# Kernel optimization log

Hardware: AMD Instinct MI355X
Metric: run time of the kernel (lower is better)

## Reference

```python
import jax, jax.numpy as jnp
import numpy as np

N_ATOMS = 20
N_IN, N_EMB_N, N_EMB_E, N_H_N, N_H_E = 4, 128, 128, 256, 256


def lstm_seq(x, Wi, bi, Wh, bh):
    """x: [B, M, T, D] -> h sequence [B, M, T, H]. Gates stacked as (i,f,g,o).
    Equivalent to the per-gate nn.Linear pairs: bi/bh are the two bias vectors."""
    B, M, T, D = x.shape
    H = Wh.shape[0]
    # precompute all input-to-hidden projections in one big GEMM: [T,B,M,4H]
    xg = jnp.einsum('bmtd,dg->tbmg', x, Wi) + bi

    def step(carry, xg_t):
        c, h = carry
        g = xg_t + h @ Wh + bh  # [B,M,4H]
        i, f, gg, o = jnp.split(g, 4, axis=-1)
        i = jax.nn.sigmoid(i)
        f = jax.nn.sigmoid(f)
        gg = jnp.tanh(gg)
        o = jax.nn.sigmoid(o)
        c = f * c + i * gg
        h = o * jnp.tanh(c)
        return (c, h), h

    z = jnp.zeros((B, M, H), x.dtype)
    _, hs = jax.lax.scan(step, (z, z), xg)  # hs: [T,B,M,H]
    return jnp.transpose(hs, (1, 2, 0, 3))


def setup_inputs() -> dict:
    key = jax.random.key(0)
    ks = jax.random.split(key, 16)
    s = 0.05
    # fully-connected directed edges without self loops -> one-hot incidence
    send, rec = np.where(~np.eye(N_ATOMS, dtype=bool))
    eye = np.eye(N_ATOMS, dtype=np.float32)
    inp = {
        'X': jax.random.normal(ks[0], (16, N_ATOMS, 64, N_IN), jnp.float32),
        'rel_rec': jnp.asarray(eye[rec]),
        'rel_send': jnp.asarray(eye[send]),
        # motion embedding fc
        'Wm': jax.random.normal(ks[1], (N_IN, N_EMB_N), jnp.float32) * s,
        'bm': jnp.zeros((N_EMB_N,), jnp.float32),
        # motion LSTM (gates i,f,g,o stacked)
        'Wmi': jax.random.normal(ks[2], (N_EMB_N, 4 * N_H_N), jnp.float32) * s,
        'bmi': jnp.zeros((4 * N_H_N,), jnp.float32),
        'Wmh': jax.random.normal(ks[3], (N_H_N, 4 * N_H_N), jnp.float32) * s,
        'bmh': jnp.zeros((4 * N_H_N,), jnp.float32),
        # interaction embedding fc (in = 2*n_h_node)
        'We': jax.random.normal(ks[4], (2 * N_H_N, N_EMB_E), jnp.float32) * s,
        'be': jnp.zeros((N_EMB_E,), jnp.float32),
        # edge LSTM
        'Wei': jax.random.normal(ks[5], (N_EMB_E, 4 * N_H_E), jnp.float32) * s,
        'bei': jnp.zeros((4 * N_H_E,), jnp.float32),
        'Weh': jax.random.normal(ks[6], (N_H_E, 4 * N_H_E), jnp.float32) * s,
        'beh': jnp.zeros((4 * N_H_E,), jnp.float32),
        # output fc
        'Wf': jax.random.normal(ks[7], (N_H_E, 1), jnp.float32) * s,
        'bf': jnp.zeros((1,), jnp.float32),
    }
    return inp


def reference(X, rel_rec, rel_send, Wm, bm, Wmi, bmi, Wmh, bmh,
              We, be, Wei, bei, Weh, beh, Wf, bf):
    # Motion embedding on temporal deltas: [B,N,T-1,n_emb_node]
    dX = X[:, :, 1:, :] - X[:, :, :-1, :]
    em = dX @ Wm + bm
    # Motion LSTM, full sequence: [B,N,T-1,Hn]
    hm = lstm_seq(em, Wmi, bmi, Wmh, bmh)
    # Interaction embedding: gather per-edge sender/receiver node states
    senders = jnp.einsum('en,bnth->beth', rel_send, hm)
    receivers = jnp.einsum('en,bnth->beth', rel_rec, hm)
    edges = jnp.concatenate([senders, receivers], axis=-1)  # [B,E,T-1,2Hn]
    ea = edges @ We + be  # [B,E,T-1,n_emb_edge]
    # Edge LSTM, last hidden state: [B,E,He]
    he = lstm_seq(ea, Wei, bei, Weh, beh)[:, :, -1, :]
    # Edge scores -> dense adjacency via incidence matrices
    A = jax.nn.sigmoid(he @ Wf + bf)[..., 0]  # [B,E]
    Ad = jnp.einsum('en,be,em->bnm', rel_send, A, rel_rec)  # send^T diag(A) rec
    return 0.5 * (Ad + jnp.transpose(Ad, (0, 2, 1)))  # symmetrize
```

## Files before the change

kernel.cpp:

```cpp
#include <hip/hip_runtime.h>
#include <stdint.h>

#define NBATCH 16
#define NNODE  20
#define TSTEPS 63
#define NEDGE  380
#define HID    256
#define RS     280

typedef __bf16 bf16x8 __attribute__((ext_vector_type(8)));
typedef float  f32x4  __attribute__((ext_vector_type(4)));

__device__ __forceinline__ float bf2f(unsigned short u){
  union { unsigned int i; float f; } v; v.i = ((unsigned int)u) << 16; return v.f;
}
__device__ __forceinline__ unsigned short f2bf(float f){
  union { float f; unsigned int i; } v; v.f = f;
  return (unsigned short)((v.i + 0x7FFFu + ((v.i >> 16) & 1u)) >> 16);
}
__device__ __forceinline__ bf16x8 as_frag(uint4 v){
  union { uint4 u; bf16x8 b; } c; c.u = v; return c.b;
}
__device__ __forceinline__ float sigmf(float x){ return 1.0f/(1.0f+__expf(-x)); }
__device__ __forceinline__ float tanh_f(float x){ float e=__expf(2.0f*x); return (e-1.0f)/(e+1.0f); }

__device__ __forceinline__ unsigned long long load_ax(const unsigned long long* p){
  return __hip_atomic_load(p, __ATOMIC_RELAXED, __HIP_MEMORY_SCOPE_AGENT);
}
__device__ __forceinline__ void store_ax(unsigned long long* p, unsigned long long v){
  __hip_atomic_store(p, v, __ATOMIC_RELAXED, __HIP_MEMORY_SCOPE_AGENT);
}
__device__ __forceinline__ void wait_vm0(){ asm volatile("s_waitcnt vmcnt(0)" ::: "memory"); }

__device__ __forceinline__ void xpose4(f32x4& v, int cl){
  float s0 = __shfl_xor((float)v[1], 1), s1 = __shfl_xor((float)v[0], 1);
  float s2 = __shfl_xor((float)v[3], 1), s3 = __shfl_xor((float)v[2], 1);
  bool b0 = (cl & 1);
  float a0 = b0 ? s0 : v[0], a1 = b0 ? v[1] : s1;
  float a2 = b0 ? s2 : v[2], a3 = b0 ? v[3] : s3;
  float t0 = __shfl_xor(a2, 2), t1 = __shfl_xor(a3, 2);
  float t2 = __shfl_xor(a0, 2), t3 = __shfl_xor(a1, 2);
  bool b1 = (cl & 2);
  v[0] = b1 ? t0 : a0; v[1] = b1 ? t1 : a1;
  v[2] = b1 ? a2 : t2; v[3] = b1 ? a3 : t3;
}

__global__ __launch_bounds__(256) void prep_a(
    const float* __restrict__ We, const float* __restrict__ Wei,
    const float* __restrict__ Wm, const float* __restrict__ Wmi,
    const float* __restrict__ bm, const float* __restrict__ bmi, const float* __restrict__ bmh,
    const float* __restrict__ be, const float* __restrict__ bei, const float* __restrict__ beh,
    float* __restrict__ Wse, float* __restrict__ Wre, float* __restrict__ WcmGI,
    float* __restrict__ bcmGI, float* __restrict__ bceGI,
    float* __restrict__ Afin, unsigned int* __restrict__ ectr, unsigned int* __restrict__ mctr){
  int bid = blockIdx.x, tid = threadIdx.x;
  if (bid < 2048){
    int idx = bid*256 + tid;
    int half = idx >> 18;
    int j = idx & 262143;
    int k = j >> 10, nn = j & 1023;
    const float* Wrow = We + (half*256 + k)*128;
    float s = 0.f;
    for (int d = 0; d < 128; ++d) s += Wrow[d] * Wei[d*1024 + nn];
    (half ? Wre : Wse)[k*1024 + nn] = s;
  } else if (bid < 2064){
    int idx = (bid-2048)*256 + tid;
    int d = idx >> 10, ci = idx & 1023;
    int col = (ci & 3)*256 + (ci >> 2);
    float s = 0.f;
    for (int j = 0; j < 128; ++j) s += Wm[d*128 + j] * Wmi[j*1024 + col];
    WcmGI[idx] = s;
  } else if (bid < 2068){
    int ci = (bid-2064)*256 + tid;
    int col = (ci & 3)*256 + (ci >> 2);
    float s = bmi[col] + bmh[col];
    for (int j = 0; j < 128; ++j) s += bm[j] * Wmi[j*1024 + col];
    bcmGI[ci] = s;
  } else if (bid < 2072){
    int ci = (bid-2068)*256 + tid;
    int col = (ci & 3)*256 + (ci >> 2);
    float s = bei[col] + beh[col];
    for (int j = 0; j < 128; ++j) s += be[j] * Wei[j*1024 + col];
    bceGI[ci] = s;
  } else if (bid == 2072){
    for (int i = tid; i < 2048; i += 256) ectr[i] = 0u;
    for (int i = tid; i < 1024; i += 256) mctr[i] = 0u;
  } else {
    int idx = (bid-2073)*256 + tid;
    if (idx < NBATCH*NEDGE) Afin[idx] = 0.f;
  }
}

__device__ __forceinline__ void pack_gi(const float* __restrict__ W,
                                        unsigned short* __restrict__ dst, int id){
  int lane = id & 63, kt = (id >> 6) & 7, tt = (id >> 9) & 1, w = (id >> 10) & 7, nb = id >> 13;
  int cl = lane & 15, q = lane >> 4;
  int gcol = (cl & 3)*256 + nb*64 + (w*2 + tt)*4 + (cl >> 2);
  int k0 = kt*32 + q*8;
  unsigned int wb[4];
  #pragma unroll
  for (int p = 0; p < 4; ++p){
    unsigned short a = f2bf(W[(k0+2*p  )*1024 + gcol]);
    unsigned short b = f2bf(W[(k0+2*p+1)*1024 + gcol]);
    wb[p] = (unsigned int)a | ((unsigned int)b << 16);
  }
  ((uint4*)dst)[id] = make_uint4(wb[0], wb[1], wb[2], wb[3]);
}

__device__ __forceinline__ void pack_one(const float* __restrict__ S,
                                         unsigned short* __restrict__ dst, int id, int n){
  int lane = id & 63, kt = (id >> 6) & 7;
  int k0 = kt*32 + ((lane >> 4) << 3);
  unsigned int wb[4];
  #pragma unroll
  for (int p = 0; p < 4; ++p){
    unsigned short a = f2bf(S[(k0+2*p  )*1024 + n]);
    unsigned short b = f2bf(S[(k0+2*p+1)*1024 + n]);
    wb[p] = (unsigned int)a | ((unsigned int)b << 16);
  }
  ((uint4*)dst)[id] = make_uint4(wb[0], wb[1], wb[2], wb[3]);
}

__global__ __launch_bounds__(256) void prep_b(
    const float* __restrict__ Wmh, const float* __restrict__ Weh,
    const float* __restrict__ Wse, const float* __restrict__ Wre,
    unsigned short* __restrict__ pWmh, unsigned short* __restrict__ pWeh,
    unsigned short* __restrict__ pWsr){
  int gid = blockIdx.x*256 + threadIdx.x;
  if (gid < 32768){
    pack_gi(Wmh, pWmh, gid);
  } else if (gid < 65536){
    pack_gi(Weh, pWeh, gid - 32768);
  } else {
    int id = gid - 65536;
    int ng = (id >> 9)*16 + (id & 15);
    const float* S = (ng < 1024) ? Wse : Wre;
    pack_one(S, pWsr, id, ng & 1023);
  }
}

__global__ __launch_bounds__(512, 2) void motion_lstm(
    const float* __restrict__ X, const float* __restrict__ WcmGI,
    const float* __restrict__ bcmGI, const unsigned short* __restrict__ pWmh,
    unsigned short* __restrict__ hm, unsigned short* __restrict__ mb,
    unsigned int* __restrict__ mctr){
  __shared__ __align__(16) unsigned short hst[16*RS];
  __shared__ float dxs[10*252];
  __shared__ __align__(16) float sWc[4*256];
  __shared__ __align__(16) float sbc[256];
  int tid = threadIdx.x, lane = tid & 63, w = tid >> 6;
  int l15 = lane & 15, quad = lane >> 4;
  int m = blockIdx.x & 31, n = blockIdx.x >> 5;
  int s0 = m*10;
  unsigned int* ctr = mctr + m*32;

  uint4 wreg[2][8];
  #pragma unroll
  for (int tt = 0; tt < 2; ++tt)
    #pragma unroll
    for (int kt = 0; kt < 8; ++kt)
      wreg[tt][kt] = ((const uint4*)pWmh)[(((n*8 + w)*2 + tt)*8 + kt)*64 + lane];

  uint4 z4 = make_uint4(0,0,0,0);
  for (int i = tid; i < 560; i += 512) ((uint4*)hst)[i] = z4;
  for (int i = tid; i < 1024; i += 512) sWc[i] = WcmGI[(i >> 8)*1024 + n*256 + (i & 255)];
  if (tid < 256) sbc[tid] = bcmGI[n*256 + tid];
  for (int i = tid; i < 2520; i += 512){
    int sl = i / 252; int r = i % 252; int t = r >> 2; int d = r & 3;
    const float* Xp = X + (((size_t)(s0 + sl)*64 + t)*4 + d);
    dxs[i] = Xp[4] - Xp[0];
  }
  __syncthreads();

  float bb[2] = { sbc[(w*2+0)*16 + l15], sbc[(w*2+1)*16 + l15] };
  int row = quad*4 + (l15 & 3);
  int hsub = l15 >> 2;
  int slr = row < 10 ? row : 9;
  float ce[2] = {0.f, 0.f};

  for (int t = 0; t < TSTEPS; ++t){
    if (t > 0){
      if (tid == 0){
        unsigned int tgt = 4u*(unsigned)t;
        while (__hip_atomic_load(ctr, __ATOMIC_RELAXED, __HIP_MEMORY_SCOPE_AGENT) < tgt)
          __builtin_amdgcn_s_sleep(1);
      }
      __syncthreads();
      const unsigned long long* mbp = (const unsigned long long*)mb
          + ((size_t)((t-1)&1)*32 + m)*16*64;
      unsigned long long pv[2]; int po[2] = {-1,-1};
      #pragma unroll
      for (int j = 0; j < 2; ++j){
        int i = tid + j*512;
        if (i < 768){
          int which = i >> 8, jj = i & 255;
          int r = jj >> 4, c = jj & 15;
          int np = which + (which >= n ? 1 : 0);
          pv[j] = load_ax(&mbp[(size_t)r*64 + np*16 + c]);
          po[j] = r*RS + np*64 + c*4;
        }
      }
      #pragma unroll
      for (int j = 0; j < 2; ++j)
        if (po[j] >= 0) *(unsigned long long*)&hst[po[j]] = pv[j];
    }
    __syncthreads();

    f32x4 acc[2];
    acc[0] = (f32x4){bb[0],bb[0],bb[0],bb[0]};
    acc[1] = (f32x4){bb[1],bb[1],bb[1],bb[1]};
    #pragma unroll
    for (int kt = 0; kt < 8; ++kt){
      bf16x8 a = as_frag(*(const uint4*)&hst[l15*RS + kt*32 + quad*8]);
      acc[0] = __builtin_amdgcn_mfma_f32_16x16x32_bf16(a, as_frag(wreg[0][kt]), acc[0], 0, 0, 0);
      acc[1] = __builtin_amdgcn_mfma_f32_16x16x32_bf16(a, as_frag(wreg[1][kt]), acc[1], 0, 0, 0);
    }
    __syncthreads();

    f32x4 dxv = *(const f32x4*)&dxs[slr*252 + t*4];
    #pragma unroll
    for (int tt = 0; tt < 2; ++tt){
      int tl = w*2 + tt;
      f32x4 v = acc[tt];
      xpose4(v, l15);
      #pragma unroll
      for (int d = 0; d < 4; ++d){
        f32x4 wv = *(const f32x4*)&sWc[d*256 + tl*16 + hsub*4];
        v[0] += dxv[d]*wv[0]; v[1] += dxv[d]*wv[1];
        v[2] += dxv[d]*wv[2]; v[3] += dxv[d]*wv[3];
      }
      float iv = sigmf(v[0]), fv = sigmf(v[1]), gg = tanh_f(v[2]), ov = sigmf(v[3]);
      float cc = fv*ce[tt] + iv*gg; ce[tt] = cc;
      hst[row*RS + n*64 + tl*4 + hsub] = f2bf(ov*tanh_f(cc));
    }
    __syncthreads();

    unsigned long long* mbc = (unsigned long long*)mb
        + ((size_t)(t&1)*32 + m)*16*64;
    if (tid < 256){
      int r = tid >> 4, c = tid & 15;
      unsigned long long v = *(const unsigned long long*)&hst[r*RS + n*64 + c*4];
      if (t < 62) store_ax(&mbc[(size_t)r*64 + n*16 + c], v);
      if (r < 10){
        int seq = s0 + r;
        int b2 = seq / 20, nd = seq - (seq/20)*20;
        *(unsigned long long*)&hm[(((size_t)(b2*63 + t)*20) + nd)*256 + n*64 + c*4] = v;
      }
    }
    wait_vm0();
    __syncthreads();
    if (t < 62 && tid == 0)
      __hip_atomic_fetch_add(ctr, 1u, __ATOMIC_RELAXED, __HIP_MEMORY_SCOPE_AGENT);
  }
}

__global__ __launch_bounds__(256) void gsr_gemm(
    const unsigned short* __restrict__ hm, const unsigned short* __restrict__ pWsr,
    unsigned short* __restrict__ gsrT){
  __shared__ __align__(16) unsigned short scol[128*100];
  int tid = threadIdx.x, lane = tid & 63, wid = tid >> 6;
  int l15 = lane & 15, quad = lane >> 4;
  int bm = blockIdx.x % 252, bn = blockIdx.x / 252;
  int rowbase = bm*80;
  f32x4 acc[5][2] = {};
  #pragma unroll
  for (int kt = 0; kt < 8; ++kt){
    bf16x8 af[5];
    #pragma unroll
    for (int mt = 0; mt < 5; ++mt)
      af[mt] = as_frag(*(const uint4*)&hm[(size_t)(rowbase + mt*16 + l15)*256 + kt*32 + quad*8]);
    #pragma unroll
    for (int j = 0; j < 2; ++j){
      int ntg = bn*8 + wid*2 + j;
      bf16x8 bfr = as_frag(*(const uint4*)&pWsr[(((size_t)ntg*8 + kt)*64 + lane)*8]);
      #pragma unroll
      for (int mt = 0; mt < 5; ++mt)
        acc[mt][j] = __builtin_amdgcn_mfma_f32_16x16x32_bf16(af[mt], bfr, acc[mt][j], 0, 0, 0);
    }
  }
  #pragma unroll
  for (int mt = 0; mt < 5; ++mt)
    #pragma unroll
    for (int j = 0; j < 2; ++j){
      int colL = (wid*2 + j)*16 + l15;
      unsigned int p0 = (unsigned)f2bf(acc[mt][j][0]) | ((unsigned)f2bf(acc[mt][j][1]) << 16);
      unsigned int p1 = (unsigned)f2bf(acc[mt][j][2]) | ((unsigned)f2bf(acc[mt][j][3]) << 16);
      *(uint2*)&scol[colL*100 + mt*16 + quad*4] = make_uint2(p0, p1);
    }
  __syncthreads();
  int half = bn >> 3;
  #pragma unroll
  for (int rep = 0; rep < 2; ++rep){
    int i = tid + rep*256;
    int btl = i >> 7, colL = i & 127;
    const unsigned short* sp = &scol[colL*100 + btl*20];
    uint2 u0 = *(const uint2*)(sp);
    uint2 u1 = *(const uint2*)(sp+4);
    uint2 u2 = *(const uint2*)(sp+8);
    uint2 u3 = *(const uint2*)(sp+12);
    uint2 u4 = *(const uint2*)(sp+16);
    unsigned short* dp = gsrT + ((size_t)(bm*4 + btl)*1024 + (bn&7)*128 + colL)*48;
    if (half){
      *(uint4*)(dp)      = make_uint4(u0.x, u0.y, u1.x, u1.y);
      *(uint4*)(dp + 8)  = make_uint4(u2.x, u2.y, u3.x, u3.y);
      *(uint2*)(dp + 16) = u4;
    } else {
      unsigned int o0 = u0.x, o1 = u0.y, o2 = u1.x & 0xffffu;
      unsigned int o3 = (u1.x >> 16) | (u1.y << 16);
      unsigned int o4 = (u1.y >> 16) | (u2.x << 16);
      unsigned int o5 = u2.x >> 16;
      unsigned int o6 = u2.y, o7 = u3.x, o8 = u3.y & 0xffffu;
      unsigned int o9 = (u3.y >> 16) | (u4.x << 16);
      unsigned int o10 = (u4.x >> 16) | (u4.y << 16);
      unsigned int o11 = u4.y >> 16;
      *(uint4*)(dp + 24) = make_uint4(o0, o1, o2, o3);
      *(uint4*)(dp + 32) = make_uint4(o4, o5, o6, o7);
      *(uint4*)(dp + 40) = make_uint4(o8, o9, o10, o11);
    }
  }
}

__device__ __forceinline__ void stage_gxb(const unsigned short* __restrict__ gsrT,
                                          unsigned short* __restrict__ gx,
                                          int tid, int b, int m, int n, int tq){
  const unsigned short* base = gsrT + (size_t)(b*63 + tq)*1024*48;
  int c = tid >> 1, chv = tid & 1;
  int g = c >> 6, hh = c & 63;
  const unsigned short* src = base + (size_t)((g << 8) + (n << 6) + hh)*48;
  unsigned short* dst = gx + (hh >> 2)*640 + (((hh & 3) << 2) + g)*40;
  if (chv == 0){
    *(uint4*)(dst)      = *(const uint4*)(src);
    *(uint4*)(dst + 8)  = *(const uint4*)(src + 8);
    *(uint2*)(dst + 16) = *(const uint2*)(src + 16);
  } else {
    const unsigned int* s3 = (const unsigned int*)(src + 24 + 6*m);
    unsigned int* d3 = (unsigned int*)(dst + 24);
    d3[0] = s3[0]; d3[1] = s3[1]; d3[2] = s3[2];
  }
}

__global__ __launch_bounds__(512, 2) void edge_lstm(
    const unsigned short* __restrict__ gsrT, const float* __restrict__ bceGI,
    const unsigned short* __restrict__ pWeh, const float* __restrict__ Wf,
    unsigned short* __restrict__ hb, float* __restrict__ Afin,
    unsigned int* __restrict__ ectr){
  __shared__ __align__(16) unsigned short hst[96*RS];
  __shared__ __align__(16) unsigned short gxb[2][10240];
  __shared__ __align__(16) float sbce[256];
  __shared__ __align__(16) float sWf[64];
  int tid = threadIdx.x, lane = tid & 63, w = tid >> 6;
  int l15 = lane & 15, quad = lane >> 4;
  int bid = blockIdx.x;
  int n = bid >> 6, G = bid & 63, b = G >> 2, m = G & 3;
  int e0 = m*95;
  unsigned int* ctr = ectr + G*32;

  uint4 wreg[2][8];
  #pragma unroll
  for (int tt = 0; tt < 2; ++tt)
    #pragma unroll
    for (int kt = 0; kt < 8; ++kt)
      wreg[tt][kt] = ((const uint4*)pWeh)[(((n*8 + w)*2 + tt)*8 + kt)*64 + lane];

  uint4 aoh[6];
  #pragma unroll
  for (int mt = 0; mt < 6; ++mt){
    int row = mt*16 + l15;
    int e = e0 + (row < 95 ? row : 94);
    int s = e / 19; int rr = e - s*19;
    int sr = s - m*5;
    int rc = rr + (rr >= s ? 1 : 0);
    unsigned int wd[4];
    #pragma unroll
    for (int p = 0; p < 4; ++p){
      int k0 = quad*8 + 2*p, k1 = k0 + 1;
      unsigned short a0 = ((k0 < 20) ? (rc == k0) : (k0 >= 24 && k0 < 29 && sr == k0-24)) ? 0x3F80 : 0;
      unsigned short a1 = ((k1 < 20) ? (rc == k1) : (k1 >= 24 && k1 < 29 && sr == k1-24)) ? 0x3F80 : 0;
      wd[p] = (unsigned int)a0 | ((unsigned int)a1 << 16);
    }
    aoh[mt] = make_uint4(wd[0], wd[1], wd[2], wd[3]);
  }

  if (tid < 256) sbce[tid] = bceGI[n*256 + tid];
  if (tid < 64)  sWf[tid]  = Wf[n*64 + tid];
  uint4 z4 = make_uint4(0,0,0,0);
  for (int i = tid; i < 3360; i += 512) ((uint4*)hst)[i] = z4;
  for (int i = tid; i < 2560; i += 512) ((uint4*)gxb)[i] = z4;
  __syncthreads();
  stage_gxb(gsrT, &gxb[0][0], tid, b, m, n, 0);
  __syncthreads();

  float bb[2]  = { sbce[(w*2+0)*16 + l15], sbce[(w*2+1)*16 + l15] };
  float wfr[2] = { sWf[(w*2+0)*4 + (l15>>2)], sWf[(w*2+1)*4 + (l15>>2)] };

  float ce[2][6]; float epi[6];
  #pragma unroll
  for (int mt = 0; mt < 6; ++mt){ ce[0][mt] = 0.f; ce[1][mt] = 0.f; epi[mt] = 0.f; }

  for (int t = 0; t < TSTEPS; ++t){
    int par = t & 1, nxt = par ^ 1;
    if (t > 0){
      if (tid == 0){
        unsigned int tgt = 4u*(unsigned)t;
        while (__hip_atomic_load(ctr, __ATOMIC_RELAXED, __HIP_MEMORY_SCOPE_AGENT) < tgt)
          __builtin_amdgcn_s_sleep(1);
      }
      __syncthreads();
      const unsigned long long* hbp = (const unsigned long long*)hb
          + (((size_t)((t-1)&1)*16 + b)*4 + m)*96*64;
      unsigned long long pv[9]; int po[9];
      #pragma unroll
      for (int j = 0; j < 9; ++j){
        int i = tid + j*512;
        int which = i / 1536, jj = i - which*1536;
        int r = jj >> 4, c = jj & 15;
        int np = which + (which >= n ? 1 : 0);
        pv[j] = load_ax(&hbp[(size_t)r*64 + np*16 + c]);
        po[j] = r*RS + np*64 + c*4;
      }
      #pragma unroll
      for (int j = 0; j < 9; ++j)
        *(unsigned long long*)&hst[po[j]] = pv[j];
    }
    if (t + 1 < TSTEPS)
      stage_gxb(gsrT, &gxb[nxt][0], tid, b, m, n, t+1);
    __syncthreads();

    f32x4 acc[2][6];
    #pragma unroll
    for (int mt = 0; mt < 6; ++mt){
      acc[0][mt] = (f32x4){bb[0],bb[0],bb[0],bb[0]};
      acc[1][mt] = (f32x4){bb[1],bb[1],bb[1],bb[1]};
    }
    #pragma unroll
    for (int kt = 0; kt < 8; ++kt){
      bf16x8 a[6];
      #pragma unroll
      for (int mt = 0; mt < 6; ++mt)
        a[mt] = as_frag(*(const uint4*)&hst[(mt*16 + l15)*RS + kt*32 + quad*8]);
      #pragma unroll
      for (int mt = 0; mt < 6; ++mt){
        acc[0][mt] = __builtin_amdgcn_mfma_f32_16x16x32_bf16(a[mt], as_frag(wreg[0][kt]), acc[0][mt], 0, 0, 0);
        acc[1][mt] = __builtin_amdgcn_mfma_f32_16x16x32_bf16(a[mt], as_frag(wreg[1][kt]), acc[1][mt], 0, 0, 0);
      }
    }
    {
      bf16x8 bx0 = as_frag(*(const uint4*)&gxb[par][(w*2+0)*640 + l15*40 + quad*8]);
      bf16x8 bx1 = as_frag(*(const uint4*)&gxb[par][(w*2+1)*640 + l15*40 + quad*8]);
      #pragma unroll
      for (int mt = 0; mt < 6; ++mt){
        acc[0][mt] = __builtin_amdgcn_mfma_f32_16x16x32_bf16(as_frag(aoh[mt]), bx0, acc[0][mt], 0, 0, 0);
        acc[1][mt] = __builtin_amdgcn_mfma_f32_16x16x32_bf16(as_frag(aoh[mt]), bx1, acc[1][mt], 0, 0, 0);
      }
    }
    __syncthreads();

    #pragma unroll
    for (int tt = 0; tt < 2; ++tt){
      int tl = w*2 + tt;
      #pragma unroll
      for (int mt = 0; mt < 6; ++mt){
        f32x4 v = acc[tt][mt];
        xpose4(v, l15);
        float iv = sigmf(v[0]), fv = sigmf(v[1]), gg = tanh_f(v[2]), ov = sigmf(v[3]);
        float cc = fv*ce[tt][mt] + iv*gg; ce[tt][mt] = cc;
        float h = ov*tanh_f(cc);
        if (t < 62){
          int row = mt*16 + quad*4 + (l15 & 3);
          hst[row*RS + n*64 + tl*4 + (l15>>2)] = f2bf(h);
        } else {
          epi[mt] += h * wfr[tt];
        }
      }
    }
    if (t < 62){
      __syncthreads();
      unsigned long long* hbc = (unsigned long long*)hb
          + (((size_t)(t&1)*16 + b)*4 + m)*96*64;
      #pragma unroll
      for (int j = 0; j < 3; ++j){
        int i = tid + j*512;
        int r = i >> 4, c = i & 15;
        unsigned long long v = *(const unsigned long long*)&hst[r*RS + n*64 + c*4];
        store_ax(&hbc[(size_t)r*64 + n*16 + c], v);
      }
      wait_vm0();
      __syncthreads();
      if (tid == 0)
        __hip_atomic_fetch_add(ctr, 1u, __ATOMIC_RELAXED, __HIP_MEMORY_SCOPE_AGENT);
    }
  }
  #pragma unroll
  for (int mt = 0; mt < 6; ++mt){
    float v = epi[mt];
    v += __shfl_xor(v, 4);
    v += __shfl_xor(v, 8);
    if (l15 < 4){
      int row = mt*16 + quad*4 + l15;
      if (row < 95)
        atomicAdd(&Afin[b*380 + e0 + row], v);
    }
  }
}

__global__ __launch_bounds__(256) void finalize(const float* __restrict__ Afin,
                                                const float* __restrict__ bfp,
                                                float* __restrict__ out){
  int idx = blockIdx.x*256 + threadIdx.x;
  if (idx >= 16*400) return;
  int b = idx / 400; int ij = idx % 400; int i = ij / 20; int j = ij % 20;
  float v = 0.f;
  if (i != j){
    int e1 = i*19 + j - (j > i ? 1 : 0);
    int e2 = j*19 + i - (i > j ? 1 : 0);
    float bf = bfp[0];
    v = 0.5f*(sigmf(Afin[b*380 + e1] + bf) + sigmf(Afin[b*380 + e2] + bf));
  }
  out[idx] = v;
}

extern "C" void kernel_launch(void* const* d_in, const int* in_sizes, int n_in,
                              void* d_out, int out_size, void* d_ws, size_t ws_size,
                              hipStream_t stream){
  (void)in_sizes; (void)n_in; (void)out_size; (void)ws_size;
  const float* X   = (const float*)d_in[0];
  const float* Wm  = (const float*)d_in[3];
  const float* bm  = (const float*)d_in[4];
  const float* Wmi = (const float*)d_in[5];
  const float* bmi = (const float*)d_in[6];
  const float* Wmh = (const float*)d_in[7];
  const float* bmh = (const float*)d_in[8];
  const float* We  = (const float*)d_in[9];
  const float* be  = (const float*)d_in[10];
  const float* Wei = (const float*)d_in[11];
  const float* bei = (const float*)d_in[12];
  const float* Weh = (const float*)d_in[13];
  const float* beh = (const float*)d_in[14];
  const float* Wf  = (const float*)d_in[15];
  const float* bfp = (const float*)d_in[16];

  char* ws = (char*)d_ws;
  float* Wse   = (float*)(ws + 0);
  float* Wre   = (float*)(ws + 1048576);
  float* WcmGI = (float*)(ws + 2097152);
  float* bcmGI = (float*)(ws + 2113536);
  float* bceGI = (float*)(ws + 2117632);
  unsigned short* pWmh = (unsigned short*)(ws + 2121728);
  unsigned short* pWeh = (unsigned short*)(ws + 2646016);
  unsigned short* pWsr = (unsigned short*)(ws + 3170304);
  unsigned short* hm   = (unsigned short*)(ws + 4218880);
  unsigned short* gsrT = (unsigned short*)(ws + 14540800);
  unsigned short* hb   = (unsigned short*)(ws + 113631232);
  unsigned short* mb   = hb;
  float* Afin          = (float*)(ws + 119922688);
  unsigned int* ectr   = (unsigned int*)(ws + 119947264);
  unsigned int* mctr   = (unsigned int*)(ws + 119955456);
  float* out = (float*)d_out;

  hipLaunchKernelGGL(prep_a, dim3(2097), dim3(256), 0, stream,
                     We, Wei, Wm, Wmi, bm, bmi, bmh, be, bei, beh,
                     Wse, Wre, WcmGI, bcmGI, bceGI, Afin, ectr, mctr);
  hipLaunchKernelGGL(prep_b, dim3(512), dim3(256), 0, stream,
                     Wmh, Weh, Wse, Wre, pWmh, pWeh, pWsr);
  {
    void* margs[] = {(void*)&X, (void*)&WcmGI, (void*)&bcmGI, (void*)&pWmh,
                     (void*)&hm, (void*)&mb, (void*)&mctr};
    hipLaunchCooperativeKernel(reinterpret_cast<void*>(motion_lstm),
                               dim3(128), dim3(512), margs, 0, stream);
  }
  hipLaunchKernelGGL(gsr_gemm, dim3(252*16), dim3(256), 0, stream,
                     hm, pWsr, gsrT);
  {
    void* eargs[] = {(void*)&gsrT, (void*)&bceGI, (void*)&pWeh, (void*)&Wf,
                     (void*)&hb, (void*)&Afin, (void*)&ectr};
    hipLaunchCooperativeKernel(reinterpret_cast<void*>(edge_lstm),
                               dim3(256), dim3(512), eargs, 0, stream);
  }
  hipLaunchKernelGGL(finalize, dim3(25), dim3(256), 0, stream,
                     Afin, bfp, out);
}
```

Before: 1.055 ms.

## Replace counter-based inter-block sync with poisoned triple-buffered data flags

Drops the per-step atomic counter, the vmcnt wait, the extra block barriers and the thread-0 spin in both LSTM kernels. Each thread instead polls its own hidden-state words in a triple-buffered exchange area until they differ from a poison pattern, and re-poisons the slot from two steps earlier. The aim is to take the barrier/flag round trip off the serial recurrence critical path. It also shrinks the gsrT sender/receiver layout from 48 to 40 columns so staging is simpler. The scheme relies on real data never equalling the poison value, and there is a bounded spin that breaks out silently.

```diff
diff --git a/kernel.cpp b/kernel.cpp
--- a/kernel.cpp
+++ b/kernel.cpp
@@ -7,6 +7,8 @@
 #define NEDGE  380
 #define HID    256
 #define RS     280
+#define SPIN_MAX (1u << 20)
+#define POISON  0xAAAAAAAAAAAAAAAAull
 
 typedef __bf16 bf16x8 __attribute__((ext_vector_type(8)));
 typedef float  f32x4  __attribute__((ext_vector_type(4)));
@@ -30,7 +32,6 @@
 __device__ __forceinline__ void store_ax(unsigned long long* p, unsigned long long v){
   __hip_atomic_store(p, v, __ATOMIC_RELAXED, __HIP_MEMORY_SCOPE_AGENT);
 }
-__device__ __forceinline__ void wait_vm0(){ asm volatile("s_waitcnt vmcnt(0)" ::: "memory"); }
 
 __device__ __forceinline__ void xpose4(f32x4& v, int cl){
   float s0 = __shfl_xor((float)v[1], 1), s1 = __shfl_xor((float)v[0], 1);
@@ -52,7 +53,7 @@
     const float* __restrict__ be, const float* __restrict__ bei, const float* __restrict__ beh,
     float* __restrict__ Wse, float* __restrict__ Wre, float* __restrict__ WcmGI,
     float* __restrict__ bcmGI, float* __restrict__ bceGI,
-    float* __restrict__ Afin, unsigned int* __restrict__ ectr, unsigned int* __restrict__ mctr){
+    float* __restrict__ Afin, uint4* __restrict__ hb3q, uint4* __restrict__ mb3q){
   int bid = blockIdx.x, tid = threadIdx.x;
   if (bid < 2048){
     int idx = bid*256 + tid;
@@ -82,12 +83,14 @@
     float s = bei[col] + beh[col];
     for (int j = 0; j < 128; ++j) s += be[j] * Wei[j*1024 + col];
     bceGI[ci] = s;
-  } else if (bid == 2072){
-    for (int i = tid; i < 2048; i += 256) ectr[i] = 0u;
-    for (int i = tid; i < 1024; i += 256) mctr[i] = 0u;
+  } else if (bid < 2096){
+    int idx = (bid-2072)*256 + tid;
+    if (idx < NBATCH*NEDGE) Afin[idx] = 0.f;
   } else {
-    int idx = (bid-2073)*256 + tid;
-    if (idx < NBATCH*NEDGE) Afin[idx] = 0.f;
+    int idx = (bid-2096)*256 + tid;
+    uint4 P = make_uint4(0xAAAAAAAAu,0xAAAAAAAAu,0xAAAAAAAAu,0xAAAAAAAAu);
+    if (idx < 589824) hb3q[idx] = P;
+    else if (idx < 638976) mb3q[idx-589824] = P;
   }
 }
 
@@ -142,8 +145,7 @@
 __global__ __launch_bounds__(512, 2) void motion_lstm(
     const float* __restrict__ X, const float* __restrict__ WcmGI,
     const float* __restrict__ bcmGI, const unsigned short* __restrict__ pWmh,
-    unsigned short* __restrict__ hm, unsigned short* __restrict__ mb,
-    unsigned int* __restrict__ mctr){
+    unsigned short* __restrict__ hm, unsigned long long* __restrict__ mb3){
   __shared__ __align__(16) unsigned short hst[16*RS];
   __shared__ float dxs[10*252];
   __shared__ __align__(16) float sWc[4*256];
@@ -152,7 +154,6 @@
   int l15 = lane & 15, quad = lane >> 4;
   int m = blockIdx.x & 31, n = blockIdx.x >> 5;
   int s0 = m*10;
-  unsigned int* ctr = mctr + m*32;
 
   uint4 wreg[2][8];
   #pragma unroll
@@ -180,15 +181,8 @@
 
   for (int t = 0; t < TSTEPS; ++t){
     if (t > 0){
-      if (tid == 0){
-        unsigned int tgt = 4u*(unsigned)t;
-        while (__hip_atomic_load(ctr, __ATOMIC_RELAXED, __HIP_MEMORY_SCOPE_AGENT) < tgt)
-          __builtin_amdgcn_s_sleep(1);
-      }
-      __syncthreads();
-      const unsigned long long* mbp = (const unsigned long long*)mb
-          + ((size_t)((t-1)&1)*32 + m)*16*64;
-      unsigned long long pv[2]; int po[2] = {-1,-1};
+      const unsigned long long* mbp = mb3 + ((size_t)((t-1)%3)*32 + m)*1024;
+      unsigned long long pv[2]; int off[2], po[2] = {-1,-1};
       #pragma unroll
       for (int j = 0; j < 2; ++j){
         int i = tid + j*512;
@@ -196,13 +190,32 @@
           int which = i >> 8, jj = i & 255;
           int r = jj >> 4, c = jj & 15;
           int np = which + (which >= n ? 1 : 0);
-          pv[j] = load_ax(&mbp[(size_t)r*64 + np*16 + c]);
-          po[j] = r*RS + np*64 + c*4;
+          off[j] = r*64 + np*16 + c;
+          po[j]  = r*RS + np*64 + c*4;
+          pv[j]  = POISON;
+        }
+      }
+      unsigned int guard = 0; bool need = true;
+      while (need){
+        need = false;
+        #pragma unroll
+        for (int j = 0; j < 2; ++j)
+          if (po[j] >= 0 && pv[j] == POISON) pv[j] = load_ax(&mbp[off[j]]);
+        #pragma unroll
+        for (int j = 0; j < 2; ++j)
+          if (po[j] >= 0 && pv[j] == POISON) need = true;
+        if (need){
+          if (++guard > SPIN_MAX) break;
+          __builtin_amdgcn_s_sleep(1);
         }
       }
       #pragma unroll
       for (int j = 0; j < 2; ++j)
         if (po[j] >= 0) *(unsigned long long*)&hst[po[j]] = pv[j];
+      if (t >= 2 && tid < 256){
+        unsigned long long* mbq = mb3 + ((size_t)((t-2)%3)*32 + m)*1024;
+        store_ax(&mbq[(size_t)(tid>>4)*64 + n*16 + (tid&15)], POISON);
+      }
     }
     __syncthreads();
 
@@ -235,22 +248,17 @@
     }
     __syncthreads();
 
-    unsigned long long* mbc = (unsigned long long*)mb
-        + ((size_t)(t&1)*32 + m)*16*64;
+    unsigned long long* mbc = mb3 + ((size_t)(t%3)*32 + m)*1024;
     if (tid < 256){
       int r = tid >> 4, c = tid & 15;
       unsigned long long v = *(const unsigned long long*)&hst[r*RS + n*64 + c*4];
       if (t < 62) store_ax(&mbc[(size_t)r*64 + n*16 + c], v);
       if (r < 10){
         int seq = s0 + r;
-        int b2 = seq / 20, nd = seq - (seq/20)*20;
+        int b2 = seq / 20, nd = seq - b2*20;
         *(unsigned long long*)&hm[(((size_t)(b2*63 + t)*20) + nd)*256 + n*64 + c*4] = v;
       }
     }
-    wait_vm0();
-    __syncthreads();
-    if (t < 62 && tid == 0)
-      __hip_atomic_fetch_add(ctr, 1u, __ATOMIC_RELAXED, __HIP_MEMORY_SCOPE_AGENT);
   }
 }
 
@@ -288,7 +296,7 @@
       *(uint2*)&scol[colL*100 + mt*16 + quad*4] = make_uint2(p0, p1);
     }
   __syncthreads();
-  int half = bn >> 3;
+  int recv = bn >> 3;
   #pragma unroll
   for (int rep = 0; rep < 2; ++rep){
     int i = tid + rep*256;
@@ -299,51 +307,44 @@
     uint2 u2 = *(const uint2*)(sp+8);
     uint2 u3 = *(const uint2*)(sp+12);
     uint2 u4 = *(const uint2*)(sp+16);
-    unsigned short* dp = gsrT + ((size_t)(bm*4 + btl)*1024 + (bn&7)*128 + colL)*48;
-    if (half){
+    unsigned short* dp = gsrT + ((size_t)(bm*4 + btl)*1024 + (bn&7)*128 + colL)*40;
+    if (recv){
       *(uint4*)(dp)      = make_uint4(u0.x, u0.y, u1.x, u1.y);
       *(uint4*)(dp + 8)  = make_uint4(u2.x, u2.y, u3.x, u3.y);
       *(uint2*)(dp + 16) = u4;
     } else {
-      unsigned int o0 = u0.x, o1 = u0.y, o2 = u1.x & 0xffffu;
-      unsigned int o3 = (u1.x >> 16) | (u1.y << 16);
-      unsigned int o4 = (u1.y >> 16) | (u2.x << 16);
-      unsigned int o5 = u2.x >> 16;
-      unsigned int o6 = u2.y, o7 = u3.x, o8 = u3.y & 0xffffu;
-      unsigned int o9 = (u3.y >> 16) | (u4.x << 16);
-      unsigned int o10 = (u4.x >> 16) | (u4.y << 16);
-      unsigned int o11 = u4.y >> 16;
-      *(uint4*)(dp + 24) = make_uint4(o0, o1, o2, o3);
-      *(uint4*)(dp + 32) = make_uint4(o4, o5, o6, o7);
-      *(uint4*)(dp + 40) = make_uint4(o8, o9, o10, o11);
+      unsigned short* dq = dp + 20;
+      *(uint2*)(dq)      = u0;
+      *(uint2*)(dq + 4)  = u1;
+      *(uint2*)(dq + 8)  = u2;
+      *(uint2*)(dq + 12) = u3;
+      *(uint2*)(dq + 16) = u4;
     }
   }
 }
 
 __device__ __forceinline__ void stage_gxb(const unsigned short* __restrict__ gsrT,
                                           unsigned short* __restrict__ gx,
-                                          int tid, int b, int m, int n, int tq){
-  const unsigned short* base = gsrT + (size_t)(b*63 + tq)*1024*48;
+                                          int tid, int b, int smin, int n, int tq){
+  const unsigned short* base = gsrT + (size_t)(b*63 + tq)*1024*40;
   int c = tid >> 1, chv = tid & 1;
   int g = c >> 6, hh = c & 63;
-  const unsigned short* src = base + (size_t)((g << 8) + (n << 6) + hh)*48;
+  const unsigned short* src = base + (size_t)((g << 8) + (n << 6) + hh)*40;
   unsigned short* dst = gx + (hh >> 2)*640 + (((hh & 3) << 2) + g)*40;
   if (chv == 0){
     *(uint4*)(dst)      = *(const uint4*)(src);
     *(uint4*)(dst + 8)  = *(const uint4*)(src + 8);
     *(uint2*)(dst + 16) = *(const uint2*)(src + 16);
   } else {
-    const unsigned int* s3 = (const unsigned int*)(src + 24 + 6*m);
-    unsigned int* d3 = (unsigned int*)(dst + 24);
-    d3[0] = s3[0]; d3[1] = s3[1]; d3[2] = s3[2];
+    const unsigned short* s3 = src + 20 + smin;
+    dst[24]=s3[0]; dst[25]=s3[1]; dst[26]=s3[2]; dst[27]=s3[3]; dst[28]=s3[4];
   }
 }
 
 __global__ __launch_bounds__(512, 2) void edge_lstm(
     const unsigned short* __restrict__ gsrT, const float* __restrict__ bceGI,
     const unsigned short* __restrict__ pWeh, const float* __restrict__ Wf,
-    unsigned short* __restrict__ hb, float* __restrict__ Afin,
-    unsigned int* __restrict__ ectr){
+    unsigned long long* __restrict__ hb3, float* __restrict__ Afin){
   __shared__ __align__(16) unsigned short hst[96*RS];
   __shared__ __align__(16) unsigned short gxb[2][10240];
   __shared__ __align__(16) float sbce[256];
@@ -353,7 +354,6 @@
   int bid = blockIdx.x;
   int n = bid >> 6, G = bid & 63, b = G >> 2, m = G & 3;
   int e0 = m*95;
-  unsigned int* ctr = ectr + G*32;
 
   uint4 wreg[2][8];
   #pragma unroll
@@ -387,7 +387,7 @@
   for (int i = tid; i < 3360; i += 512) ((uint4*)hst)[i] = z4;
   for (int i = tid; i < 2560; i += 512) ((uint4*)gxb)[i] = z4;
   __syncthreads();
-  stage_gxb(gsrT, &gxb[0][0], tid, b, m, n, 0);
+  stage_gxb(gsrT, &gxb[0][0], tid, b, m*5, n, 0);
   __syncthreads();
 
   float bb[2]  = { sbce[(w*2+0)*16 + l15], sbce[(w*2+1)*16 + l15] };
@@ -400,30 +400,46 @@
   for (int t = 0; t < TSTEPS; ++t){
     int par = t & 1, nxt = par ^ 1;
     if (t > 0){
-      if (tid == 0){
-        unsigned int tgt = 4u*(unsigned)t;
-        while (__hip_atomic_load(ctr, __ATOMIC_RELAXED, __HIP_MEMORY_SCOPE_AGENT) < tgt)
-          __builtin_amdgcn_s_sleep(1);
-      }
-      __syncthreads();
-      const unsigned long long* hbp = (const unsigned long long*)hb
-          + (((size_t)((t-1)&1)*16 + b)*4 + m)*96*64;
-      unsigned long long pv[9]; int po[9];
+      const unsigned long long* hbp = hb3 + ((size_t)((t-1)%3)*64 + G)*6144;
+      unsigned long long pv[9]; int off[9]; int po[9];
       #pragma unroll
       for (int j = 0; j < 9; ++j){
         int i = tid + j*512;
         int which = i / 1536, jj = i - which*1536;
         int r = jj >> 4, c = jj & 15;
         int np = which + (which >= n ? 1 : 0);
-        pv[j] = load_ax(&hbp[(size_t)r*64 + np*16 + c]);
-        po[j] = r*RS + np*64 + c*4;
+        off[j] = r*64 + np*16 + c;
+        po[j]  = r*RS + np*64 + c*4;
+        pv[j]  = POISON;
+      }
+      unsigned int guard = 0; bool need = true;
+      while (need){
+        need = false;
+        #pragma unroll
+        for (int j = 0; j < 9; ++j)
+          if (pv[j] == POISON) pv[j] = load_ax(&hbp[off[j]]);
+        #pragma unroll
+        for (int j = 0; j < 9; ++j)
+          if (pv[j] == POISON) need = true;
+        if (need){
+          if (++guard > SPIN_MAX) break;
+          __builtin_amdgcn_s_sleep(1);
+        }
       }
       #pragma unroll
       for (int j = 0; j < 9; ++j)
         *(unsigned long long*)&hst[po[j]] = pv[j];
+      if (t >= 2){
+        unsigned long long* hbq = hb3 + ((size_t)((t-2)%3)*64 + G)*6144;
+        #pragma unroll
+        for (int j = 0; j < 3; ++j){
+          int i = tid + j*512;
+          store_ax(&hbq[(size_t)(i>>4)*64 + n*16 + (i&15)], POISON);
+        }
+      }
     }
     if (t + 1 < TSTEPS)
-      stage_gxb(gsrT, &gxb[nxt][0], tid, b, m, n, t+1);
+      stage_gxb(gsrT, &gxb[nxt][0], tid, b, m*5, n, t+1);
     __syncthreads();
 
     f32x4 acc[2][6];
@@ -475,19 +491,13 @@
     }
     if (t < 62){
       __syncthreads();
-      unsigned long long* hbc = (unsigned long long*)hb
-          + (((size_t)(t&1)*16 + b)*4 + m)*96*64;
+      unsigned long long* hbc = hb3 + ((size_t)(t%3)*64 + G)*6144;
       #pragma unroll
       for (int j = 0; j < 3; ++j){
         int i = tid + j*512;
-        int r = i >> 4, c = i & 15;
-        unsigned long long v = *(const unsigned long long*)&hst[r*RS + n*64 + c*4];
-        store_ax(&hbc[(size_t)r*64 + n*16 + c], v);
-      }
-      wait_vm0();
-      __syncthreads();
-      if (tid == 0)
-        __hip_atomic_fetch_add(ctr, 1u, __ATOMIC_RELAXED, __HIP_MEMORY_SCOPE_AGENT);
+        unsigned long long v = *(const unsigned long long*)&hst[(i>>4)*RS + n*64 + (i&15)*4];
+        store_ax(&hbc[(size_t)(i>>4)*64 + n*16 + (i&15)], v);
+      }
     }
   }
   #pragma unroll
@@ -550,21 +560,20 @@
   unsigned short* pWsr = (unsigned short*)(ws + 3170304);
   unsigned short* hm   = (unsigned short*)(ws + 4218880);
   unsigned short* gsrT = (unsigned short*)(ws + 14540800);
-  unsigned short* hb   = (unsigned short*)(ws + 113631232);
-  unsigned short* mb   = hb;
-  float* Afin          = (float*)(ws + 119922688);
-  unsigned int* ectr   = (unsigned int*)(ws + 119947264);
-  unsigned int* mctr   = (unsigned int*)(ws + 119955456);
+  unsigned long long* hb3 = (unsigned long long*)(ws + 97116160);
+  float* Afin          = (float*)(ws + 106553344);
+  unsigned long long* mb3 = (unsigned long long*)gsrT;
   float* out = (float*)d_out;
 
-  hipLaunchKernelGGL(prep_a, dim3(2097), dim3(256), 0, stream,
+  hipLaunchKernelGGL(prep_a, dim3(4592), dim3(256), 0, stream,
                      We, Wei, Wm, Wmi, bm, bmi, bmh, be, bei, beh,
-                     Wse, Wre, WcmGI, bcmGI, bceGI, Afin, ectr, mctr);
+                     Wse, Wre, WcmGI, bcmGI, bceGI, Afin,
+                     (uint4*)hb3, (uint4*)mb3);
   hipLaunchKernelGGL(prep_b, dim3(512), dim3(256), 0, stream,
                      Wmh, Weh, Wse, Wre, pWmh, pWeh, pWsr);
   {
     void* margs[] = {(void*)&X, (void*)&WcmGI, (void*)&bcmGI, (void*)&pWmh,
-                     (void*)&hm, (void*)&mb, (void*)&mctr};
+                     (void*)&hm, (void*)&mb3};
     hipLaunchCooperativeKernel(reinterpret_cast<void*>(motion_lstm),
                                dim3(128), dim3(512), margs, 0, stream);
   }
@@ -572,7 +581,7 @@
                      hm, pWsr, gsrT);
   {
     void* eargs[] = {(void*)&gsrT, (void*)&bceGI, (void*)&pWeh, (void*)&Wf,
-                     (void*)&hb, (void*)&Afin, (void*)&ectr};
+                     (void*)&hb3, (void*)&Afin};
     hipLaunchCooperativeKernel(reinterpret_cast<void*>(edge_lstm),
                                dim3(256), dim3(512), eargs, 0, stream);
   }
```

Result: no change. 1.066 ms (+1.0%).
